# Optimization experiments

Hardware: AMD Instinct MI355X
Metric: run time of the kernel (lower is better)

Reference implementation:

```python
import jax, jax.numpy as jnp
import numpy as np

jax.config.update("jax_enable_x64", True)

# --- static config (matches init_kwargs) ---
L = 6            # voxel_level_num
F = 8            # feature_dim
T = 524288       # per-level feature table size
B = 4194304      # buffer_size (hash table size)
N = 1048576      # number of query points
LEAF = 0.25      # leaf_voxel_size
UP = 2.0         # up_scale_factor

PRIMES = jnp.array([73856093, 19349669, 83492791], dtype=jnp.int64)
# corner offsets, z varies fastest (same order as torch self.steps)
STEPS = jnp.array([[0,0,0],[0,0,1],[0,1,0],[0,1,1],
                   [1,0,0],[1,0,1],[1,1,0],[1,1,1]], dtype=jnp.float32)


def setup_inputs() -> dict:
    key = jax.random.key(0)
    k1, k2, k3, k4 = jax.random.split(key, 4)
    query_points = jax.random.uniform(k1, (N, 3), dtype=jnp.float32) * 50.0
    features = 0.01 * jax.random.normal(k2, (L, T, F), dtype=jnp.float32)
    idx = jax.random.randint(k3, (L, B), 0, T, dtype=jnp.int64)
    empty = jax.random.uniform(k4, (L, B)) < 0.2
    feature_indexs = jnp.where(empty, jnp.int64(-1), idx)
    return {"query_points": query_points, "features": features,
            "feature_indexs": feature_indexs}


def _trilinear_coeffs(d):
    # d: [N,3] fractional coords in the cell; order matches STEPS (z fastest)
    tx, ty, tz = d[:, 0], d[:, 1], d[:, 2]
    return jnp.stack([
        (1-tx)*(1-ty)*(1-tz), (1-tx)*(1-ty)*tz,
        (1-tx)*ty*(1-tz),     (1-tx)*ty*tz,
        tx*(1-ty)*(1-tz),     tx*(1-ty)*tz,
        tx*ty*(1-tz),         tx*ty*tz,
    ], axis=1)  # [N,8]


def reference(query_points, features, feature_indexs):
    out = jnp.zeros((query_points.shape[0], F), dtype=query_points.dtype)
    for i in range(L):  # small fixed level loop (structurally distinct resolutions)
        res = LEAF * (UP ** i)
        scaled = query_points / res                      # [N,3]
        base = jnp.floor(scaled)
        corners = (base[:, None, :] + STEPS[None]).astype(jnp.int64)  # [N,8,3]
        keys = jnp.mod((corners * PRIMES).sum(-1), B)    # [N,8] spatial hash
        idx = feature_indexs[i][keys]                    # [N,8] gather, -1 = empty
        valid = idx.min(axis=1) > -1                     # [N] all 8 corners allocated
        coeffs = _trilinear_coeffs(scaled - base)        # [N,8]
        feats = features[i][jnp.clip(idx, 0, T - 1)]     # [N,8,F] gather
        level = jnp.einsum('nkf,nk->nf', feats, coeffs)  # trilinear interp
        out = out + jnp.where(valid[:, None], level, jnp.zeros((), out.dtype))
    return out
```

## Files before the change

### kernel.cpp

```cpp
#include <hip/hip_runtime.h>


static constexpr int      NPTS  = 1048576;
static constexpr int      NF    = 8;
static constexpr int      TTAB  = 524288;
static constexpr unsigned BTAB  = 4194304u;
static constexpr unsigned BMASK = BTAB - 1u;
static constexpr unsigned P0 = 73856093u, P1 = 19349669u, P2 = 83492791u;

static constexpr int NBIN = 4096;
static constexpr int SB   = 256;
static constexpr int PPB  = NPTS / SB;
static constexpr int ITER = PPB / 256;
static constexpr int BCAP = 512;

static constexpr int S2 = 51, S3 = 26, S4 = 14, S5 = 8;
static constexpr int OCC2 = 0, OCC3 = OCC2 + S2*S2, OCC4 = OCC3 + S3*S3,
                     OCC5 = OCC4 + S4*S4, OCCW = OCC5 + S5*S5;
static constexpr int CB2 = 0, CB3 = CB2 + (S2-1)*(S2-1),
                     CB4 = CB3 + (S3-1)*(S3-1), CB5 = CB4 + (S4-1)*(S4-1),
                     CBW = CB5 + (S5-1)*(S5-1);

static constexpr int RB2 = (S2*S2+3)/4, RB3 = (S3*S3+3)/4,
                     RB4 = (S4*S4+3)/4, RB5 = (S5*S5+3)/4;
static constexpr int OCCB = RB2+RB3+RB4+RB5;

static constexpr size_t SORTED_BYTES = (size_t)NPTS * 16;
static constexpr size_t OCC_OFF = SORTED_BYTES;
static constexpr size_t CB_OFF  = OCC_OFF + (size_t)OCCW * 8;
static constexpr size_t BB_OFF  = CB_OFF  + (size_t)CBW  * 8;
static constexpr size_t WS_FULL = BB_OFF + (size_t)NBIN * 4;

typedef float f4 __attribute__((ext_vector_type(4)));

__device__ __forceinline__ void nhv_point_g(
    float qx, float qy, float qz,
    const float* __restrict__ feat, const int* __restrict__ fidx,
    const unsigned long long* __restrict__ cbit, float acc[NF])
{
    float fx01[2], fy01[2], fz01[2];
    unsigned h01[2];
#pragma unroll
    for (int i = 0; i < 2; ++i) {
        const float inv = (i == 0) ? 4.0f : 2.0f;
        const float sx = qx*inv, sy = qy*inv, sz = qz*inv;
        const float bx = floorf(sx), by = floorf(sy), bz = floorf(sz);
        fx01[i] = sx-bx; fy01[i] = sy-by; fz01[i] = sz-bz;
        h01[i] = (unsigned)(int)bx*P0 + (unsigned)(int)by*P1 + (unsigned)(int)bz*P2;
    }
    int id0[8], id1[8];
#pragma unroll
    for (int k = 0; k < 8; ++k) {
        unsigned key = h01[0];
        if (k & 4) key += P0;
        if (k & 2) key += P1;
        if (k & 1) key += P2;
        id0[k] = fidx[key & BMASK];
    }
#pragma unroll
    for (int k = 0; k < 8; ++k) {
        unsigned key = h01[1];
        if (k & 4) key += P0;
        if (k & 2) key += P1;
        if (k & 1) key += P2;
        id1[k] = fidx[BTAB + (key & BMASK)];
    }

    float fxh[4], fyh[4], fzh[4];
    int   ixh[4], iyh[4], izh[4];
    unsigned vhi = 0;
    const int Ss[4]  = {S2, S3, S4, S5};
    const int CBo[4] = {CB2, CB3, CB4, CB5};
#pragma unroll
    for (int j = 0; j < 4; ++j) {
        const float inv = 1.0f / (float)(1 << j);
        const float sx = qx*inv, sy = qy*inv, sz = qz*inv;
        const float bx = floorf(sx), by = floorf(sy), bz = floorf(sz);
        fxh[j] = sx-bx; fyh[j] = sy-by; fzh[j] = sz-bz;
        ixh[j] = (int)bx; iyh[j] = (int)by; izh[j] = (int)bz;
        const int C = Ss[j] - 1;
        const unsigned long long row = cbit[CBo[j] + izh[j]*C + iyh[j]];
        vhi |= (unsigned)((row >> ixh[j]) & 1ull) << j;
    }

#pragma unroll
    for (int f = 0; f < NF; ++f) acc[f] = 0.0f;

    {
        int mn = id0[0];
#pragma unroll
        for (int k = 1; k < 8; ++k) mn = min(mn, id0[k]);
        if (mn > -1) {
            const float wxv[2] = {1.0f - fx01[0], fx01[0]};
            const float wyv[2] = {1.0f - fy01[0], fy01[0]};
            const float wzv[2] = {1.0f - fz01[0], fz01[0]};
#pragma unroll
            for (int k = 0; k < 8; ++k) {
                const float c = wxv[(k>>2)&1] * wyv[(k>>1)&1] * wzv[k&1];
                const float4* p = (const float4*)(feat + (size_t)id0[k] * NF);
                const float4 lo = p[0], hi = p[1];
                acc[0]+=c*lo.x; acc[1]+=c*lo.y; acc[2]+=c*lo.z; acc[3]+=c*lo.w;
                acc[4]+=c*hi.x; acc[5]+=c*hi.y; acc[6]+=c*hi.z; acc[7]+=c*hi.w;
            }
        }
    }
    {
        int mn = id1[0];
#pragma unroll
        for (int k = 1; k < 8; ++k) mn = min(mn, id1[k]);
        if (mn > -1) {
            const float wxv[2] = {1.0f - fx01[1], fx01[1]};
            const float wyv[2] = {1.0f - fy01[1], fy01[1]};
            const float wzv[2] = {1.0f - fz01[1], fz01[1]};
            const float* __restrict__ fb = feat + (size_t)(TTAB * NF);
#pragma unroll
            for (int k = 0; k < 8; ++k) {
                const float c = wxv[(k>>2)&1] * wyv[(k>>1)&1] * wzv[k&1];
                const float4* p = (const float4*)(fb + (size_t)id1[k] * NF);
                const float4 lo = p[0], hi = p[1];
                acc[0]+=c*lo.x; acc[1]+=c*lo.y; acc[2]+=c*lo.z; acc[3]+=c*lo.w;
                acc[4]+=c*hi.x; acc[5]+=c*hi.y; acc[6]+=c*hi.z; acc[7]+=c*hi.w;
            }
        }
    }
#pragma unroll
    for (int j = 0; j < 4; ++j) {
        if (vhi & (1u << j)) {
            const int lvl = 2 + j;
            const unsigned h = (unsigned)ixh[j]*P0 + (unsigned)iyh[j]*P1
                             + (unsigned)izh[j]*P2;
            const int* __restrict__ tab = fidx + (size_t)lvl * BTAB;
            int id[8];
#pragma unroll
            for (int k = 0; k < 8; ++k) {
                unsigned key = h;
                if (k & 4) key += P0;
                if (k & 2) key += P1;
                if (k & 1) key += P2;
                id[k] = tab[key & BMASK];
            }
            const float wxv[2] = {1.0f - fxh[j], fxh[j]};
            const float wyv[2] = {1.0f - fyh[j], fyh[j]};
            const float wzv[2] = {1.0f - fzh[j], fzh[j]};
            const float* __restrict__ fb = feat + (size_t)lvl * (TTAB * NF);
#pragma unroll
            for (int k = 0; k < 8; ++k) {
                const float c = wxv[(k>>2)&1] * wyv[(k>>1)&1] * wzv[k&1];
                const float4* p = (const float4*)(fb + (size_t)id[k] * NF);
                const float4 lo = p[0], hi = p[1];
                acc[0]+=c*lo.x; acc[1]+=c*lo.y; acc[2]+=c*lo.z; acc[3]+=c*lo.w;
                acc[4]+=c*hi.x; acc[5]+=c*hi.y; acc[6]+=c*hi.z; acc[7]+=c*hi.w;
            }
        }
    }
}

__device__ __forceinline__ void nhv_point(
    float qx, float qy, float qz,
    const float* __restrict__ feat, const int* __restrict__ fidx, float acc[NF])
{
    float fx[6], fy[6], fz[6];
    unsigned h[6];
#pragma unroll
    for (int i = 0; i < 6; ++i) {
        const float inv = 4.0f / (float)(1 << i);
        const float sx = qx*inv, sy = qy*inv, sz = qz*inv;
        const float bx = floorf(sx), by = floorf(sy), bz = floorf(sz);
        fx[i] = sx-bx; fy[i] = sy-by; fz[i] = sz-bz;
        h[i] = (unsigned)(int)bx*P0 + (unsigned)(int)by*P1 + (unsigned)(int)bz*P2;
    }
    int id[6][8];
#pragma unroll
    for (int i = 0; i < 6; ++i) {
        const int* __restrict__ tab = fidx + (size_t)i * BTAB;
#pragma unroll
        for (int k = 0; k < 8; ++k) {
            unsigned key = h[i];
            if (k & 4) key += P0;
            if (k & 2) key += P1;
            if (k & 1) key += P2;
            id[i][k] = tab[key & BMASK];
        }
    }
#pragma unroll
    for (int f = 0; f < NF; ++f) acc[f] = 0.0f;
#pragma unroll
    for (int i = 0; i < 6; ++i) {
        int mn = id[i][0];
#pragma unroll
        for (int k = 1; k < 8; ++k) mn = min(mn, id[i][k]);
        if (mn > -1) {
            const float wxv[2] = {1.0f - fx[i], fx[i]};
            const float wyv[2] = {1.0f - fy[i], fy[i]};
            const float wzv[2] = {1.0f - fz[i], fz[i]};
            const float* __restrict__ fb = feat + (size_t)i * (TTAB * NF);
#pragma unroll
            for (int k = 0; k < 8; ++k) {
                const float c = wxv[(k>>2)&1] * wyv[(k>>1)&1] * wzv[k&1];
                const float4* p = (const float4*)(fb + (size_t)id[i][k] * NF);
                const float4 lo = p[0], hi = p[1];
                acc[0]+=c*lo.x; acc[1]+=c*lo.y; acc[2]+=c*lo.z; acc[3]+=c*lo.w;
                acc[4]+=c*hi.x; acc[5]+=c*hi.y; acc[6]+=c*hi.z; acc[7]+=c*hi.w;
            }
        }
    }
}

__device__ __forceinline__ unsigned expand4(unsigned v) {
    return (v & 1u) | ((v & 2u) << 2) | ((v & 4u) << 4) | ((v & 8u) << 6);
}
__device__ __forceinline__ unsigned bin_of(float x, float y, float z) {
    unsigned bx = min(15u, (unsigned)(int)(x * 0.32f));
    unsigned by = min(15u, (unsigned)(int)(y * 0.32f));
    unsigned bz = min(15u, (unsigned)(int)(z * 0.32f));
    return expand4(bx) | (expand4(by) << 1) | (expand4(bz) << 2);
}

__global__ __launch_bounds__(256) void pre_k(const int* __restrict__ fidx,
                                             unsigned long long* __restrict__ occ,
                                             const float* __restrict__ qp,
                                             unsigned* __restrict__ hist) {
    __shared__ unsigned lh[NBIN];
    const int t = threadIdx.x, b = blockIdx.x;
    if (b < OCCB) {
        int lvl, S, occoff, bb = b;
        if (bb < RB2)              { lvl = 2; S = S2; occoff = OCC2; }
        else if ((bb -= RB2) < RB3){ lvl = 3; S = S3; occoff = OCC3; }
        else if ((bb -= RB3) < RB4){ lvl = 4; S = S4; occoff = OCC4; }
        else        { bb -= RB4;     lvl = 5; S = S5; occoff = OCC5; }
        const int row  = bb * 4 + (t >> 6);
        const int lane = t & 63;
        if (row < S * S) {
            const int y = row % S, z = row / S;
            bool v = false;
            if (lane < S) {
                const unsigned key = ((unsigned)lane*P0 + (unsigned)y*P1
                                    + (unsigned)z*P2) & BMASK;
                v = fidx[(size_t)lvl * BTAB + key] >= 0;
            }
            const unsigned long long m = __ballot(v);
            if (lane == 0) occ[occoff + row] = m;
        }
    } else {
        const int bh = b - OCCB;
        for (int i = t; i < NBIN; i += 256) lh[i] = 0u;
        __syncthreads();
        const int base = bh * PPB;
#pragma unroll
        for (int i = 0; i < ITER; ++i) {
            const int p = base + i * 256 + t;
            atomicAdd(&lh[bin_of(qp[3*p], qp[3*p+1], qp[3*p+2])], 1u);
        }
        __syncthreads();
        for (int i = t; i < NBIN; i += 256) hist[(size_t)bh * NBIN + i] = lh[i];
    }
}

__global__ __launch_bounds__(256) void mid_k(unsigned* __restrict__ hist,
                                             unsigned* __restrict__ binbase,
                                             const unsigned long long* __restrict__ occ,
                                             unsigned long long* __restrict__ cbit) {
    const int t = threadIdx.x, b = blockIdx.x;
    if (b < 16) {
        const int bin = b * 256 + t;
        unsigned run = 0;
        for (int blk = 0; blk < SB; ++blk) {
            const unsigned v = hist[(size_t)blk * NBIN + bin];
            hist[(size_t)blk * NBIN + bin] = run;
            run += v;
        }
        binbase[bin] = run;
    } else {
        const int cr = (b - 16) * 256 + t;
        if (cr >= CBW) return;
        int S, occoff, cboff, local;
        if (cr < CB3)      { S = S2; occoff = OCC2; cboff = CB2; local = cr; }
        else if (cr < CB4) { S = S3; occoff = OCC3; cboff = CB3; local = cr - CB3; }
        else if (cr < CB5) { S = S4; occoff = OCC4; cboff = CB4; local = cr - CB4; }
        else               { S = S5; occoff = OCC5; cboff = CB5; local = cr - CB5; }
        const int C = S - 1;
        const int cy = local % C, cz = local / C;
        const unsigned long long r00 = occ[occoff +  cz      * S + cy    ];
        const unsigned long long r10 = occ[occoff +  cz      * S + cy + 1];
        const unsigned long long r01 = occ[occoff + (cz + 1) * S + cy    ];
        const unsigned long long r11 = occ[occoff + (cz + 1) * S + cy + 1];
        const unsigned long long cw = (r00 & (r00 >> 1)) & (r10 & (r10 >> 1))
                                    & (r01 & (r01 >> 1)) & (r11 & (r11 >> 1));
        cbit[cboff + cz * C + cy] = cw;
    }
}

__global__ __launch_bounds__(256) void binscan_k(unsigned* __restrict__ binbase) {
    __shared__ unsigned tot[256];
    const int t = threadIdx.x;
    unsigned v[16];
    unsigned s = 0;
#pragma unroll
    for (int i = 0; i < 16; ++i) { v[i] = s; s += binbase[t * 16 + i]; }
    tot[t] = s;
    __syncthreads();
    for (int d = 1; d < 256; d <<= 1) {
        const unsigned x = (t >= d) ? tot[t - d] : 0u;
        __syncthreads();
        tot[t] += x;
        __syncthreads();
    }
    const unsigned cb = tot[t] - s;
#pragma unroll
    for (int i = 0; i < 16; ++i) binbase[t * 16 + i] = cb + v[i];
}

__global__ __launch_bounds__(256) void scatter_k(const float* __restrict__ qp,
                                                 const unsigned* __restrict__ hist,
                                                 const unsigned* __restrict__ binbase,
                                                 float4* __restrict__ sorted) {
    __shared__ unsigned cur[NBIN];
    const int b = blockIdx.x, t = threadIdx.x;
    for (int i = t; i < NBIN; i += 256)
        cur[i] = binbase[i] + hist[(size_t)b * NBIN + i];
    __syncthreads();
    const int base = b * PPB;
#pragma unroll
    for (int i = 0; i < ITER; ++i) {
        const int p = base + i * 256 + t;
        const float x = qp[3*p], y = qp[3*p+1], z = qp[3*p+2];
        const unsigned slot = atomicAdd(&cur[bin_of(x, y, z)], 1u);
        sorted[slot] = make_float4(x, y, z, __uint_as_float((unsigned)p));
    }
}

__global__ __launch_bounds__(256) void binsort_k(float4* __restrict__ sorted,
                                                 const unsigned* __restrict__ binbase) {
    __shared__ float4        pts[BCAP];
    __shared__ unsigned char sk[BCAP];
    __shared__ unsigned      cnt[64];
    const int bin = blockIdx.x, t = threadIdx.x;
    const unsigned start = binbase[bin];
    const unsigned end   = (bin < NBIN - 1) ? binbase[bin + 1] : (unsigned)NPTS;
    const int n = (int)(end - start);
    if (n <= 1 || n > BCAP) return;

    if (t < 64) cnt[t] = 0u;
    __syncthreads();
#pragma unroll
    for (int r = 0; r < BCAP / 256; ++r) {
        const int i = r * 256 + t;
        if (i < n) {
            const float4 p = sorted[start + i];
            pts[i] = p;
            const unsigned ux = (unsigned)(int)(p.x * 1.28f) & 3u;
            const unsigned uy = (unsigned)(int)(p.y * 1.28f) & 3u;
            const unsigned uz = (unsigned)(int)(p.z * 1.28f) & 3u;
            const unsigned s = (ux & 1u) | ((uy & 1u) << 1) | ((uz & 1u) << 2)
                             | ((ux >> 1) << 3) | ((uy >> 1) << 4) | ((uz >> 1) << 5);
            sk[i] = (unsigned char)s;
            atomicAdd(&cnt[s], 1u);
        }
    }
    __syncthreads();
    if (t == 0) {
        unsigned run = 0;
#pragma unroll
        for (int i = 0; i < 64; ++i) { const unsigned v = cnt[i]; cnt[i] = run; run += v; }
    }
    __syncthreads();
#pragma unroll
    for (int r = 0; r < BCAP / 256; ++r) {
        const int i = r * 256 + t;
        if (i < n) {
            const unsigned dest = atomicAdd(&cnt[sk[i]], 1u);
            sorted[start + dest] = pts[i];
        }
    }
}

__global__ __launch_bounds__(256) void nhv_main_k(
    const float4* __restrict__ sp, const float* __restrict__ feat,
    const int* __restrict__ fidx, const unsigned long long* __restrict__ cbit,
    float* __restrict__ out)
{
    const int nwg = NPTS / 256;
    const int bid = blockIdx.x;
    const int swz = (bid & 7) * (nwg >> 3) + (bid >> 3);
    const int j   = swz * 256 + (int)threadIdx.x;

    const f4 s = __builtin_nontemporal_load((const f4*)sp + j);
    float acc[NF];
    nhv_point_g(s.x, s.y, s.z, feat, fidx, cbit, acc);
    const unsigned n = __float_as_uint(s.w);
    f4* o = (f4*)(out + (size_t)n * NF);
    f4 lo = {acc[0], acc[1], acc[2], acc[3]};
    f4 hi = {acc[4], acc[5], acc[6], acc[7]};
    __builtin_nontemporal_store(lo, o);
    __builtin_nontemporal_store(hi, o + 1);
}

__global__ __launch_bounds__(256) void nhv_direct_k(
    const float* __restrict__ qp, const float* __restrict__ feat,
    const int* __restrict__ fidx, float* __restrict__ out)
{
    const int n = blockIdx.x * 256 + threadIdx.x;
    if (n >= NPTS) return;
    float acc[NF];
    nhv_point(qp[3*n], qp[3*n+1], qp[3*n+2], feat, fidx, acc);
    float4* o = (float4*)(out + (size_t)n * NF);
    o[0] = make_float4(acc[0], acc[1], acc[2], acc[3]);
    o[1] = make_float4(acc[4], acc[5], acc[6], acc[7]);
}

extern "C" void kernel_launch(void* const* d_in, const int* in_sizes, int n_in,
                              void* d_out, int out_size, void* d_ws, size_t ws_size,
                              hipStream_t stream) {
    const float* qp   = (const float*)d_in[0];
    const float* feat = (const float*)d_in[1];
    const int*   fidx = (const int*)d_in[2];
    float*       out  = (float*)d_out;

    if (ws_size >= WS_FULL) {
        float4*             sorted  = (float4*)d_ws;
        unsigned long long* occ     = (unsigned long long*)((char*)d_ws + OCC_OFF);
        unsigned long long* cbit    = (unsigned long long*)((char*)d_ws + CB_OFF);
        unsigned*           binbase = (unsigned*)((char*)d_ws + BB_OFF);
        unsigned*           hist    = (unsigned*)d_out;

        hipLaunchKernelGGL(pre_k,    dim3(OCCB + SB), dim3(256), 0, stream,
                           fidx, occ, qp, hist);
        hipLaunchKernelGGL(mid_k,    dim3(16 + (CBW + 255) / 256), dim3(256), 0, stream,
                           hist, binbase, occ, cbit);
        hipLaunchKernelGGL(binscan_k, dim3(1),    dim3(256), 0, stream, binbase);
        hipLaunchKernelGGL(scatter_k, dim3(SB),   dim3(256), 0, stream,
                           qp, hist, binbase, sorted);
        hipLaunchKernelGGL(binsort_k, dim3(NBIN), dim3(256), 0, stream, sorted, binbase);
        hipLaunchKernelGGL(nhv_main_k, dim3(NPTS/256), dim3(256), 0, stream,
                           sorted, feat, fidx, cbit, out);
    } else {
        hipLaunchKernelGGL(nhv_direct_k, dim3(NPTS/256), dim3(256), 0, stream,
                           qp, feat, fidx, out);
    }
}
```

Before: 197.9 us.

## Split level evaluation into two passes for fine and coarse levels

The single main kernel is split into two kernels. The first computes only levels 0 and 1 and writes partial sums to a workspace buffer, or to the output if there is not enough workspace. The second reloads those partials and adds levels 2 to 5. The aim is to keep each pass's working set (hash tables and feature tables) smaller so it hits cache more often. It also switches the preprocessing loads and stores to nontemporal hints. The cost is an extra kernel launch and an extra write and read of 32 bytes per point.

```diff
diff --git a/kernel.cpp b/kernel.cpp
--- a/kernel.cpp
+++ b/kernel.cpp
@@ -20,7 +20,6 @@
 static constexpr int CB2 = 0, CB3 = CB2 + (S2-1)*(S2-1),
                      CB4 = CB3 + (S3-1)*(S3-1), CB5 = CB4 + (S4-1)*(S4-1),
                      CBW = CB5 + (S5-1)*(S5-1);
-
 static constexpr int RB2 = (S2*S2+3)/4, RB3 = (S3*S3+3)/4,
                      RB4 = (S4*S4+3)/4, RB5 = (S5*S5+3)/4;
 static constexpr int OCCB = RB2+RB3+RB4+RB5;
@@ -29,14 +28,15 @@
 static constexpr size_t OCC_OFF = SORTED_BYTES;
 static constexpr size_t CB_OFF  = OCC_OFF + (size_t)OCCW * 8;
 static constexpr size_t BB_OFF  = CB_OFF  + (size_t)CBW  * 8;
-static constexpr size_t WS_FULL = BB_OFF + (size_t)NBIN * 4;
+static constexpr size_t WS_MIN  = BB_OFF + (size_t)NBIN * 4;
+static constexpr size_t ACC_OFF = (WS_MIN + 255) & ~(size_t)255;
+static constexpr size_t WS_ACC  = ACC_OFF + (size_t)NPTS * NF * 4;
 
 typedef float f4 __attribute__((ext_vector_type(4)));
 
-__device__ __forceinline__ void nhv_point_g(
+__device__ __forceinline__ void nhv_lvl01(
     float qx, float qy, float qz,
-    const float* __restrict__ feat, const int* __restrict__ fidx,
-    const unsigned long long* __restrict__ cbit, float acc[NF])
+    const float* __restrict__ feat, const int* __restrict__ fidx, float acc[NF])
 {
     float fx01[2], fy01[2], fz01[2];
     unsigned h01[2];
@@ -65,7 +65,50 @@
         if (k & 1) key += P2;
         id1[k] = fidx[BTAB + (key & BMASK)];
     }
-
+    {
+        int mn = id0[0];
+#pragma unroll
+        for (int k = 1; k < 8; ++k) mn = min(mn, id0[k]);
+        if (mn > -1) {
+            const float wxv[2] = {1.0f - fx01[0], fx01[0]};
+            const float wyv[2] = {1.0f - fy01[0], fy01[0]};
+            const float wzv[2] = {1.0f - fz01[0], fz01[0]};
+#pragma unroll
+            for (int k = 0; k < 8; ++k) {
+                const float c = wxv[(k>>2)&1] * wyv[(k>>1)&1] * wzv[k&1];
+                const float4* p = (const float4*)(feat + (size_t)id0[k] * NF);
+                const float4 lo = p[0], hi = p[1];
+                acc[0]+=c*lo.x; acc[1]+=c*lo.y; acc[2]+=c*lo.z; acc[3]+=c*lo.w;
+                acc[4]+=c*hi.x; acc[5]+=c*hi.y; acc[6]+=c*hi.z; acc[7]+=c*hi.w;
+            }
+        }
+    }
+    {
+        int mn = id1[0];
+#pragma unroll
+        for (int k = 1; k < 8; ++k) mn = min(mn, id1[k]);
+        if (mn > -1) {
+            const float wxv[2] = {1.0f - fx01[1], fx01[1]};
+            const float wyv[2] = {1.0f - fy01[1], fy01[1]};
+            const float wzv[2] = {1.0f - fz01[1], fz01[1]};
+            const float* __restrict__ fb = feat + (size_t)(TTAB * NF);
+#pragma unroll
+            for (int k = 0; k < 8; ++k) {
+                const float c = wxv[(k>>2)&1] * wyv[(k>>1)&1] * wzv[k&1];
+                const float4* p = (const float4*)(fb + (size_t)id1[k] * NF);
+                const float4 lo = p[0], hi = p[1];
+                acc[0]+=c*lo.x; acc[1]+=c*lo.y; acc[2]+=c*lo.z; acc[3]+=c*lo.w;
+                acc[4]+=c*hi.x; acc[5]+=c*hi.y; acc[6]+=c*hi.z; acc[7]+=c*hi.w;
+            }
+        }
+    }
+}
+
+__device__ __forceinline__ void nhv_lvl25(
+    float qx, float qy, float qz,
+    const float* __restrict__ feat, const int* __restrict__ fidx,
+    const unsigned long long* __restrict__ cbit, float acc[NF])
+{
     float fxh[4], fyh[4], fzh[4];
     int   ixh[4], iyh[4], izh[4];
     unsigned vhi = 0;
@@ -81,47 +124,6 @@
         const int C = Ss[j] - 1;
         const unsigned long long row = cbit[CBo[j] + izh[j]*C + iyh[j]];
         vhi |= (unsigned)((row >> ixh[j]) & 1ull) << j;
-    }
-
-#pragma unroll
-    for (int f = 0; f < NF; ++f) acc[f] = 0.0f;
-
-    {
-        int mn = id0[0];
-#pragma unroll
-        for (int k = 1; k < 8; ++k) mn = min(mn, id0[k]);
-        if (mn > -1) {
-            const float wxv[2] = {1.0f - fx01[0], fx01[0]};
-            const float wyv[2] = {1.0f - fy01[0], fy01[0]};
-            const float wzv[2] = {1.0f - fz01[0], fz01[0]};
-#pragma unroll
-            for (int k = 0; k < 8; ++k) {
-                const float c = wxv[(k>>2)&1] * wyv[(k>>1)&1] * wzv[k&1];
-                const float4* p = (const float4*)(feat + (size_t)id0[k] * NF);
-                const float4 lo = p[0], hi = p[1];
-                acc[0]+=c*lo.x; acc[1]+=c*lo.y; acc[2]+=c*lo.z; acc[3]+=c*lo.w;
-                acc[4]+=c*hi.x; acc[5]+=c*hi.y; acc[6]+=c*hi.z; acc[7]+=c*hi.w;
-            }
-        }
-    }
-    {
-        int mn = id1[0];
-#pragma unroll
-        for (int k = 1; k < 8; ++k) mn = min(mn, id1[k]);
-        if (mn > -1) {
-            const float wxv[2] = {1.0f - fx01[1], fx01[1]};
-            const float wyv[2] = {1.0f - fy01[1], fy01[1]};
-            const float wzv[2] = {1.0f - fz01[1], fz01[1]};
-            const float* __restrict__ fb = feat + (size_t)(TTAB * NF);
-#pragma unroll
-            for (int k = 0; k < 8; ++k) {
-                const float c = wxv[(k>>2)&1] * wyv[(k>>1)&1] * wzv[k&1];
-                const float4* p = (const float4*)(fb + (size_t)id1[k] * NF);
-                const float4 lo = p[0], hi = p[1];
-                acc[0]+=c*lo.x; acc[1]+=c*lo.y; acc[2]+=c*lo.z; acc[3]+=c*lo.w;
-                acc[4]+=c*hi.x; acc[5]+=c*hi.y; acc[6]+=c*hi.z; acc[7]+=c*hi.w;
-            }
-        }
     }
 #pragma unroll
     for (int j = 0; j < 4; ++j) {
@@ -249,10 +251,14 @@
 #pragma unroll
         for (int i = 0; i < ITER; ++i) {
             const int p = base + i * 256 + t;
-            atomicAdd(&lh[bin_of(qp[3*p], qp[3*p+1], qp[3*p+2])], 1u);
+            const float x = __builtin_nontemporal_load(qp + 3*p);
+            const float y = __builtin_nontemporal_load(qp + 3*p + 1);
+            const float z = __builtin_nontemporal_load(qp + 3*p + 2);
+            atomicAdd(&lh[bin_of(x, y, z)], 1u);
         }
         __syncthreads();
-        for (int i = t; i < NBIN; i += 256) hist[(size_t)bh * NBIN + i] = lh[i];
+        for (int i = t; i < NBIN; i += 256)
+            __builtin_nontemporal_store(lh[i], hist + (size_t)bh * NBIN + i);
     }
 }
 
@@ -323,9 +329,12 @@
 #pragma unroll
     for (int i = 0; i < ITER; ++i) {
         const int p = base + i * 256 + t;
-        const float x = qp[3*p], y = qp[3*p+1], z = qp[3*p+2];
+        const float x = __builtin_nontemporal_load(qp + 3*p);
+        const float y = __builtin_nontemporal_load(qp + 3*p + 1);
+        const float z = __builtin_nontemporal_load(qp + 3*p + 2);
         const unsigned slot = atomicAdd(&cur[bin_of(x, y, z)], 1u);
-        sorted[slot] = make_float4(x, y, z, __uint_as_float((unsigned)p));
+        const f4 v = {x, y, z, __uint_as_float((unsigned)p)};
+        __builtin_nontemporal_store(v, (f4*)sorted + slot);
     }
 }
 
@@ -346,7 +355,8 @@
     for (int r = 0; r < BCAP / 256; ++r) {
         const int i = r * 256 + t;
         if (i < n) {
-            const float4 p = sorted[start + i];
+            const f4 pv = __builtin_nontemporal_load((const f4*)sorted + (start + i));
+            const float4 p = make_float4(pv.x, pv.y, pv.z, pv.w);
             pts[i] = p;
             const unsigned ux = (unsigned)(int)(p.x * 1.28f) & 3u;
             const unsigned uy = (unsigned)(int)(p.y * 1.28f) & 3u;
@@ -369,14 +379,17 @@
         const int i = r * 256 + t;
         if (i < n) {
             const unsigned dest = atomicAdd(&cnt[sk[i]], 1u);
-            sorted[start + dest] = pts[i];
-        }
-    }
-}
-
-__global__ __launch_bounds__(256) void nhv_main_k(
+            const float4 p = pts[i];
+            const f4 v = {p.x, p.y, p.z, p.w};
+            __builtin_nontemporal_store(v, (f4*)sorted + (start + dest));
+        }
+    }
+}
+
+template<bool USE_WS>
+__global__ __launch_bounds__(256) void phA_k(
     const float4* __restrict__ sp, const float* __restrict__ feat,
-    const int* __restrict__ fidx, const unsigned long long* __restrict__ cbit,
+    const int* __restrict__ fidx, float* __restrict__ accbuf,
     float* __restrict__ out)
 {
     const int nwg = NPTS / 256;
@@ -385,9 +398,54 @@
     const int j   = swz * 256 + (int)threadIdx.x;
 
     const f4 s = __builtin_nontemporal_load((const f4*)sp + j);
+    float acc[NF] = {0.f,0.f,0.f,0.f,0.f,0.f,0.f,0.f};
+    nhv_lvl01(s.x, s.y, s.z, feat, fidx, acc);
+
+    f4 lo = {acc[0], acc[1], acc[2], acc[3]};
+    f4 hi = {acc[4], acc[5], acc[6], acc[7]};
+    if (USE_WS) {
+        f4* o = (f4*)(accbuf + (size_t)j * NF);
+        __builtin_nontemporal_store(lo, o);
+        __builtin_nontemporal_store(hi, o + 1);
+    } else {
+        const unsigned n = __float_as_uint(s.w);
+        f4* o = (f4*)(out + (size_t)n * NF);
+        __builtin_nontemporal_store(lo, o);
+        __builtin_nontemporal_store(hi, o + 1);
+    }
+}
+
+template<bool USE_WS>
+__global__ __launch_bounds__(256) void phB_k(
+    const float4* __restrict__ sp, const float* __restrict__ feat,
+    const int* __restrict__ fidx, const unsigned long long* __restrict__ cbit,
+    const float* __restrict__ accbuf, float* __restrict__ out)
+{
+    const int nwg = NPTS / 256;
+    const int bid = blockIdx.x;
+    const int swz = (bid & 7) * (nwg >> 3) + (bid >> 3);
+    const int j   = swz * 256 + (int)threadIdx.x;
+
+    const f4 s = __builtin_nontemporal_load((const f4*)sp + j);
+    const unsigned n = __float_as_uint(s.w);
+
     float acc[NF];
-    nhv_point_g(s.x, s.y, s.z, feat, fidx, cbit, acc);
-    const unsigned n = __float_as_uint(s.w);
+    if (USE_WS) {
+        const f4* a = (const f4*)(accbuf + (size_t)j * NF);
+        const f4 lo = __builtin_nontemporal_load(a);
+        const f4 hi = __builtin_nontemporal_load(a + 1);
+        acc[0]=lo.x; acc[1]=lo.y; acc[2]=lo.z; acc[3]=lo.w;
+        acc[4]=hi.x; acc[5]=hi.y; acc[6]=hi.z; acc[7]=hi.w;
+    } else {
+        const f4* a = (const f4*)(out + (size_t)n * NF);
+        const f4 lo = __builtin_nontemporal_load(a);
+        const f4 hi = __builtin_nontemporal_load(a + 1);
+        acc[0]=lo.x; acc[1]=lo.y; acc[2]=lo.z; acc[3]=lo.w;
+        acc[4]=hi.x; acc[5]=hi.y; acc[6]=hi.z; acc[7]=hi.w;
+    }
+
+    nhv_lvl25(s.x, s.y, s.z, feat, fidx, cbit, acc);
+
     f4* o = (f4*)(out + (size_t)n * NF);
     f4 lo = {acc[0], acc[1], acc[2], acc[3]};
     f4 hi = {acc[4], acc[5], acc[6], acc[7]};
@@ -416,25 +474,28 @@
     const int*   fidx = (const int*)d_in[2];
     float*       out  = (float*)d_out;
 
-    if (ws_size >= WS_FULL) {
+    if (ws_size >= WS_MIN) {
         float4*             sorted  = (float4*)d_ws;
         unsigned long long* occ     = (unsigned long long*)((char*)d_ws + OCC_OFF);
         unsigned long long* cbit    = (unsigned long long*)((char*)d_ws + CB_OFF);
         unsigned*           binbase = (unsigned*)((char*)d_ws + BB_OFF);
         unsigned*           hist    = (unsigned*)d_out;
 
-        hipLaunchKernelGGL(pre_k,    dim3(OCCB + SB), dim3(256), 0, stream,
-                           fidx, occ, qp, hist);
-        hipLaunchKernelGGL(mid_k,    dim3(16 + (CBW + 255) / 256), dim3(256), 0, stream,
-                           hist, binbase, occ, cbit);
-        hipLaunchKernelGGL(binscan_k, dim3(1),    dim3(256), 0, stream, binbase);
-        hipLaunchKernelGGL(scatter_k, dim3(SB),   dim3(256), 0, stream,
-                           qp, hist, binbase, sorted);
-        hipLaunchKernelGGL(binsort_k, dim3(NBIN), dim3(256), 0, stream, sorted, binbase);
-        hipLaunchKernelGGL(nhv_main_k, dim3(NPTS/256), dim3(256), 0, stream,
-                           sorted, feat, fidx, cbit, out);
+        pre_k<<<dim3(OCCB + SB), dim3(256), 0, stream>>>(fidx, occ, qp, hist);
+        mid_k<<<dim3(16 + (CBW + 255) / 256), dim3(256), 0, stream>>>(hist, binbase, occ, cbit);
+        binscan_k<<<dim3(1), dim3(256), 0, stream>>>(binbase);
+        scatter_k<<<dim3(SB), dim3(256), 0, stream>>>(qp, hist, binbase, sorted);
+        binsort_k<<<dim3(NBIN), dim3(256), 0, stream>>>(sorted, binbase);
+
+        if (ws_size >= WS_ACC) {
+            float* accbuf = (float*)((char*)d_ws + ACC_OFF);
+            phA_k<true><<<dim3(NPTS/256), dim3(256), 0, stream>>>(sorted, feat, fidx, accbuf, out);
+            phB_k<true><<<dim3(NPTS/256), dim3(256), 0, stream>>>(sorted, feat, fidx, cbit, accbuf, out);
+        } else {
+            phA_k<false><<<dim3(NPTS/256), dim3(256), 0, stream>>>(sorted, feat, fidx, nullptr, out);
+            phB_k<false><<<dim3(NPTS/256), dim3(256), 0, stream>>>(sorted, feat, fidx, cbit, nullptr, out);
+        }
     } else {
-        hipLaunchKernelGGL(nhv_direct_k, dim3(NPTS/256), dim3(256), 0, stream,
-                           qp, feat, fidx, out);
-    }
-}
+        nhv_direct_k<<<dim3(NPTS/256), dim3(256), 0, stream>>>(qp, feat, fidx, out);
+    }
+}
```

Result: slower. 276.7 us (+39.8%).

## Precompute validity bitmaps for levels 0-1 to skip index gathers on invalid cells

Applied to the files above, without the earlier changes.

Adds a pre-pass that packs the level 0 and 1 hash-slot validity (index >= 0) into a 1-bit-per-slot bitmap, which is 1 MiB total. The main kernel first tests all 8 corners against this small, cache-friendly bitmap and only gathers the 32-bit indices and features when every corner is valid. This is meant to cut random 4-byte gathers into the 16 MiB-per-level index table, since with about 20% empty slots only about 17% of cells are fully valid. In exchange the pre-pass streams two full index levels (32 MiB), and several loads and stores are switched to nontemporal hints.

```diff
diff --git a/kernel.cpp b/kernel.cpp
--- a/kernel.cpp
+++ b/kernel.cpp
@@ -20,23 +20,28 @@
 static constexpr int CB2 = 0, CB3 = CB2 + (S2-1)*(S2-1),
                      CB4 = CB3 + (S3-1)*(S3-1), CB5 = CB4 + (S4-1)*(S4-1),
                      CBW = CB5 + (S5-1)*(S5-1);
-
 static constexpr int RB2 = (S2*S2+3)/4, RB3 = (S3*S3+3)/4,
                      RB4 = (S4*S4+3)/4, RB5 = (S5*S5+3)/4;
 static constexpr int OCCB = RB2+RB3+RB4+RB5;
 
+static constexpr int BM01W = 2 * (int)(BTAB / 32);
+static constexpr int BM01B = BM01W / 256;
+
 static constexpr size_t SORTED_BYTES = (size_t)NPTS * 16;
-static constexpr size_t OCC_OFF = SORTED_BYTES;
-static constexpr size_t CB_OFF  = OCC_OFF + (size_t)OCCW * 8;
-static constexpr size_t BB_OFF  = CB_OFF  + (size_t)CBW  * 8;
-static constexpr size_t WS_FULL = BB_OFF + (size_t)NBIN * 4;
+static constexpr size_t OCC_OFF  = SORTED_BYTES;
+static constexpr size_t CB_OFF   = OCC_OFF + (size_t)OCCW * 8;
+static constexpr size_t BB_OFF   = CB_OFF  + (size_t)CBW  * 8;
+static constexpr size_t BM01_OFF = (BB_OFF + (size_t)NBIN * 4 + 255) & ~(size_t)255;
+static constexpr size_t WS_FULL  = BM01_OFF + (size_t)BM01W * 4;
 
 typedef float f4 __attribute__((ext_vector_type(4)));
+typedef int   i4 __attribute__((ext_vector_type(4)));
 
 __device__ __forceinline__ void nhv_point_g(
     float qx, float qy, float qz,
     const float* __restrict__ feat, const int* __restrict__ fidx,
-    const unsigned long long* __restrict__ cbit, float acc[NF])
+    const unsigned long long* __restrict__ cbit,
+    const unsigned* __restrict__ bm01, float acc[NF])
 {
     float fx01[2], fy01[2], fz01[2];
     unsigned h01[2];
@@ -48,22 +53,21 @@
         fx01[i] = sx-bx; fy01[i] = sy-by; fz01[i] = sz-bz;
         h01[i] = (unsigned)(int)bx*P0 + (unsigned)(int)by*P1 + (unsigned)(int)bz*P2;
     }
-    int id0[8], id1[8];
-#pragma unroll
-    for (int k = 0; k < 8; ++k) {
-        unsigned key = h01[0];
-        if (k & 4) key += P0;
-        if (k & 2) key += P1;
-        if (k & 1) key += P2;
-        id0[k] = fidx[key & BMASK];
-    }
-#pragma unroll
-    for (int k = 0; k < 8; ++k) {
-        unsigned key = h01[1];
-        if (k & 4) key += P0;
-        if (k & 2) key += P1;
-        if (k & 1) key += P2;
-        id1[k] = fidx[BTAB + (key & BMASK)];
+    unsigned v01 = 0;
+#pragma unroll
+    for (int i = 0; i < 2; ++i) {
+        const unsigned* __restrict__ bl = bm01 + (size_t)i * (BTAB / 32);
+        unsigned vv = ~0u;
+#pragma unroll
+        for (int k = 0; k < 8; ++k) {
+            unsigned key = h01[i];
+            if (k & 4) key += P0;
+            if (k & 2) key += P1;
+            if (k & 1) key += P2;
+            key &= BMASK;
+            vv &= (bl[key >> 5] >> (key & 31u));
+        }
+        v01 |= (vv & 1u) << i;
     }
 
     float fxh[4], fyh[4], fzh[4];
@@ -86,37 +90,27 @@
 #pragma unroll
     for (int f = 0; f < NF; ++f) acc[f] = 0.0f;
 
-    {
-        int mn = id0[0];
-#pragma unroll
-        for (int k = 1; k < 8; ++k) mn = min(mn, id0[k]);
-        if (mn > -1) {
-            const float wxv[2] = {1.0f - fx01[0], fx01[0]};
-            const float wyv[2] = {1.0f - fy01[0], fy01[0]};
-            const float wzv[2] = {1.0f - fz01[0], fz01[0]};
+#pragma unroll
+    for (int i = 0; i < 2; ++i) {
+        if (v01 & (1u << i)) {
+            const int* __restrict__ tab = fidx + (size_t)i * BTAB;
+            int id[8];
+#pragma unroll
+            for (int k = 0; k < 8; ++k) {
+                unsigned key = h01[i];
+                if (k & 4) key += P0;
+                if (k & 2) key += P1;
+                if (k & 1) key += P2;
+                id[k] = tab[key & BMASK];
+            }
+            const float wxv[2] = {1.0f - fx01[i], fx01[i]};
+            const float wyv[2] = {1.0f - fy01[i], fy01[i]};
+            const float wzv[2] = {1.0f - fz01[i], fz01[i]};
+            const float* __restrict__ fb = feat + (size_t)i * (TTAB * NF);
 #pragma unroll
             for (int k = 0; k < 8; ++k) {
                 const float c = wxv[(k>>2)&1] * wyv[(k>>1)&1] * wzv[k&1];
-                const float4* p = (const float4*)(feat + (size_t)id0[k] * NF);
-                const float4 lo = p[0], hi = p[1];
-                acc[0]+=c*lo.x; acc[1]+=c*lo.y; acc[2]+=c*lo.z; acc[3]+=c*lo.w;
-                acc[4]+=c*hi.x; acc[5]+=c*hi.y; acc[6]+=c*hi.z; acc[7]+=c*hi.w;
-            }
-        }
-    }
-    {
-        int mn = id1[0];
-#pragma unroll
-        for (int k = 1; k < 8; ++k) mn = min(mn, id1[k]);
-        if (mn > -1) {
-            const float wxv[2] = {1.0f - fx01[1], fx01[1]};
-            const float wyv[2] = {1.0f - fy01[1], fy01[1]};
-            const float wzv[2] = {1.0f - fz01[1], fz01[1]};
-            const float* __restrict__ fb = feat + (size_t)(TTAB * NF);
-#pragma unroll
-            for (int k = 0; k < 8; ++k) {
-                const float c = wxv[(k>>2)&1] * wyv[(k>>1)&1] * wzv[k&1];
-                const float4* p = (const float4*)(fb + (size_t)id1[k] * NF);
+                const float4* p = (const float4*)(fb + (size_t)id[k] * NF);
                 const float4 lo = p[0], hi = p[1];
                 acc[0]+=c*lo.x; acc[1]+=c*lo.y; acc[2]+=c*lo.z; acc[3]+=c*lo.w;
                 acc[4]+=c*hi.x; acc[5]+=c*hi.y; acc[6]+=c*hi.z; acc[7]+=c*hi.w;
@@ -218,6 +212,7 @@
 
 __global__ __launch_bounds__(256) void pre_k(const int* __restrict__ fidx,
                                              unsigned long long* __restrict__ occ,
+                                             unsigned* __restrict__ bm01,
                                              const float* __restrict__ qp,
                                              unsigned* __restrict__ hist) {
     __shared__ unsigned lh[NBIN];
@@ -241,18 +236,35 @@
             const unsigned long long m = __ballot(v);
             if (lane == 0) occ[occoff + row] = m;
         }
+    } else if (b < OCCB + BM01B) {
+        const int g = (b - OCCB) * 256 + t;
+        const i4* p = (const i4*)(fidx + (size_t)g * 32);
+        unsigned w = 0;
+#pragma unroll
+        for (int j = 0; j < 8; ++j) {
+            const i4 v = __builtin_nontemporal_load(p + j);
+            w |= (unsigned)(v.x >= 0) << (4 * j + 0);
+            w |= (unsigned)(v.y >= 0) << (4 * j + 1);
+            w |= (unsigned)(v.z >= 0) << (4 * j + 2);
+            w |= (unsigned)(v.w >= 0) << (4 * j + 3);
+        }
+        bm01[g] = w;
     } else {
-        const int bh = b - OCCB;
+        const int bh = b - OCCB - BM01B;
         for (int i = t; i < NBIN; i += 256) lh[i] = 0u;
         __syncthreads();
         const int base = bh * PPB;
 #pragma unroll
         for (int i = 0; i < ITER; ++i) {
             const int p = base + i * 256 + t;
-            atomicAdd(&lh[bin_of(qp[3*p], qp[3*p+1], qp[3*p+2])], 1u);
+            const float x = __builtin_nontemporal_load(qp + 3*p);
+            const float y = __builtin_nontemporal_load(qp + 3*p + 1);
+            const float z = __builtin_nontemporal_load(qp + 3*p + 2);
+            atomicAdd(&lh[bin_of(x, y, z)], 1u);
         }
         __syncthreads();
-        for (int i = t; i < NBIN; i += 256) hist[(size_t)bh * NBIN + i] = lh[i];
+        for (int i = t; i < NBIN; i += 256)
+            __builtin_nontemporal_store(lh[i], hist + (size_t)bh * NBIN + i);
     }
 }
 
@@ -323,9 +335,12 @@
 #pragma unroll
     for (int i = 0; i < ITER; ++i) {
         const int p = base + i * 256 + t;
-        const float x = qp[3*p], y = qp[3*p+1], z = qp[3*p+2];
+        const float x = __builtin_nontemporal_load(qp + 3*p);
+        const float y = __builtin_nontemporal_load(qp + 3*p + 1);
+        const float z = __builtin_nontemporal_load(qp + 3*p + 2);
         const unsigned slot = atomicAdd(&cur[bin_of(x, y, z)], 1u);
-        sorted[slot] = make_float4(x, y, z, __uint_as_float((unsigned)p));
+        const f4 v = {x, y, z, __uint_as_float((unsigned)p)};
+        __builtin_nontemporal_store(v, (f4*)sorted + slot);
     }
 }
 
@@ -346,7 +361,8 @@
     for (int r = 0; r < BCAP / 256; ++r) {
         const int i = r * 256 + t;
         if (i < n) {
-            const float4 p = sorted[start + i];
+            const f4 pv = __builtin_nontemporal_load((const f4*)sorted + (start + i));
+            const float4 p = make_float4(pv.x, pv.y, pv.z, pv.w);
             pts[i] = p;
             const unsigned ux = (unsigned)(int)(p.x * 1.28f) & 3u;
             const unsigned uy = (unsigned)(int)(p.y * 1.28f) & 3u;
@@ -369,7 +385,9 @@
         const int i = r * 256 + t;
         if (i < n) {
             const unsigned dest = atomicAdd(&cnt[sk[i]], 1u);
-            sorted[start + dest] = pts[i];
+            const float4 p = pts[i];
+            const f4 v = {p.x, p.y, p.z, p.w};
+            __builtin_nontemporal_store(v, (f4*)sorted + (start + dest));
         }
     }
 }
@@ -377,7 +395,7 @@
 __global__ __launch_bounds__(256) void nhv_main_k(
     const float4* __restrict__ sp, const float* __restrict__ feat,
     const int* __restrict__ fidx, const unsigned long long* __restrict__ cbit,
-    float* __restrict__ out)
+    const unsigned* __restrict__ bm01, float* __restrict__ out)
 {
     const int nwg = NPTS / 256;
     const int bid = blockIdx.x;
@@ -386,7 +404,7 @@
 
     const f4 s = __builtin_nontemporal_load((const f4*)sp + j);
     float acc[NF];
-    nhv_point_g(s.x, s.y, s.z, feat, fidx, cbit, acc);
+    nhv_point_g(s.x, s.y, s.z, feat, fidx, cbit, bm01, acc);
     const unsigned n = __float_as_uint(s.w);
     f4* o = (f4*)(out + (size_t)n * NF);
     f4 lo = {acc[0], acc[1], acc[2], acc[3]};
@@ -421,20 +439,16 @@
         unsigned long long* occ     = (unsigned long long*)((char*)d_ws + OCC_OFF);
         unsigned long long* cbit    = (unsigned long long*)((char*)d_ws + CB_OFF);
         unsigned*           binbase = (unsigned*)((char*)d_ws + BB_OFF);
+        unsigned*           bm01    = (unsigned*)((char*)d_ws + BM01_OFF);
         unsigned*           hist    = (unsigned*)d_out;
 
-        hipLaunchKernelGGL(pre_k,    dim3(OCCB + SB), dim3(256), 0, stream,
-                           fidx, occ, qp, hist);
-        hipLaunchKernelGGL(mid_k,    dim3(16 + (CBW + 255) / 256), dim3(256), 0, stream,
-                           hist, binbase, occ, cbit);
-        hipLaunchKernelGGL(binscan_k, dim3(1),    dim3(256), 0, stream, binbase);
-        hipLaunchKernelGGL(scatter_k, dim3(SB),   dim3(256), 0, stream,
-                           qp, hist, binbase, sorted);
-        hipLaunchKernelGGL(binsort_k, dim3(NBIN), dim3(256), 0, stream, sorted, binbase);
-        hipLaunchKernelGGL(nhv_main_k, dim3(NPTS/256), dim3(256), 0, stream,
-                           sorted, feat, fidx, cbit, out);
+        pre_k<<<dim3(OCCB + BM01B + SB), dim3(256), 0, stream>>>(fidx, occ, bm01, qp, hist);
+        mid_k<<<dim3(16 + (CBW + 255) / 256), dim3(256), 0, stream>>>(hist, binbase, occ, cbit);
+        binscan_k<<<dim3(1), dim3(256), 0, stream>>>(binbase);
+        scatter_k<<<dim3(SB), dim3(256), 0, stream>>>(qp, hist, binbase, sorted);
+        binsort_k<<<dim3(NBIN), dim3(256), 0, stream>>>(sorted, binbase);
+        nhv_main_k<<<dim3(NPTS/256), dim3(256), 0, stream>>>(sorted, feat, fidx, cbit, bm01, out);
     } else {
-        hipLaunchKernelGGL(nhv_direct_k, dim3(NPTS/256), dim3(256), 0, stream,
-                           qp, feat, fidx, out);
-    }
-}
+        nhv_direct_k<<<dim3(NPTS/256), dim3(256), 0, stream>>>(qp, feat, fidx, out);
+    }
+}
```

After: 213.9 us. 8.1% more time.
